# Kernel optimization log

Hardware: AMD Instinct MI355X
Metric: run time of the kernel (lower is better)

The kernel has to match this reference:

```python
import jax, jax.numpy as jnp
import numpy as np

B, C, N, E, F = 8, 4, 2048, 512, 2048
EPS = 1e-5
MASK_SCALE = 5.0


def layer_norm(x, gamma, beta):
    mu = jnp.mean(x, axis=-1, keepdims=True)
    var = jnp.mean(jnp.square(x - mu), axis=-1, keepdims=True)
    return (x - mu) * jax.lax.rsqrt(var + EPS) * gamma + beta


def setup_inputs() -> dict:
    key = jax.random.key(0)
    ks = jax.random.split(key, 8)
    src = jax.random.normal(ks[0], (B, C, N, E), dtype=jnp.float32)
    key_padding_mask = jax.random.uniform(ks[1], (B, N), dtype=jnp.float32)
    # FFN params (torch Linear default init scale ~ U(-1/sqrt(fan_in), +))
    W1 = jax.random.normal(ks[2], (E, F), dtype=jnp.float32) / np.sqrt(E)
    b1 = jnp.zeros((F,), dtype=jnp.float32)
    W2 = jax.random.normal(ks[3], (F, E), dtype=jnp.float32) / np.sqrt(F)
    b2 = jnp.zeros((E,), dtype=jnp.float32)
    g1 = jnp.ones((E,), dtype=jnp.float32)
    be1 = jnp.zeros((E,), dtype=jnp.float32)
    g2 = jnp.ones((E,), dtype=jnp.float32)
    be2 = jnp.zeros((E,), dtype=jnp.float32)
    return {"src": src, "key_padding_mask": key_padding_mask,
            "W1": W1, "b1": b1, "W2": W2, "b2": b2,
            "g1": g1, "be1": be1, "g2": g2, "be2": be2}


def reference(src, key_padding_mask, W1, b1, W2, b2, g1, be1, g2, be2):
    # src: [B, C, N, E]; channels batched into one fused attention call
    scale = 1.0 / jnp.sqrt(jnp.asarray(src.shape[-1], src.dtype))
    scores = jnp.einsum('bcne,bcme->bcnm', src, src) * scale  # [B,C,N,N]
    scores = scores - key_padding_mask[:, None, None, :] * MASK_SCALE
    attn = jax.nn.softmax(scores, axis=-1)
    attn_out = jnp.einsum('bcnm,bcme->bcne', attn, src)
    # residual + norm1 (dropout is identity at eval)
    src2 = layer_norm(src + attn_out, g1, be1)
    # feedforward: Linear -> ReLU -> Linear
    ff = jax.nn.relu(jnp.einsum('bcne,ef->bcnf', src2, W1) + b1)
    ff = jnp.einsum('bcnf,fe->bcne', ff, W2) + b2
    out = layer_norm(src2 + ff, g2, be2)
    return out
```

## Files before the change

kernel.cpp:

```cpp
#include <hip/hip_runtime.h>
#include <stdint.h>

constexpr int CB = 8, CC = 4, CN = 2048, CE = 512, CF = 2048;
constexpr long long TOT = (long long)CB * CC * CN * CE;
constexpr int G = 4;
constexpr int MCH = 32768;
constexpr float SCALE = 0.04419417382415922f;
constexpr float MASK_SCALE = 5.0f;
constexpr float EPS = 1e-5f;

typedef unsigned short bf16_t;
typedef __attribute__((ext_vector_type(4))) float f32x4;
typedef __attribute__((ext_vector_type(8))) short s16x8;

#define DEV static __device__ __forceinline__

DEV unsigned short f2bf(float f) {
    unsigned u = __float_as_uint(f);
    unsigned r = (u + 0x7fffu + ((u >> 16) & 1u)) >> 16;
    return (unsigned short)r;
}
DEV float bf2f(unsigned short b) {
    return __uint_as_float(((unsigned)b) << 16);
}

typedef const __attribute__((address_space(1))) unsigned int* gptr_t;
typedef __attribute__((address_space(3))) unsigned int* lptr_t;
DEV void async16(const void* g, void* l) {
    __builtin_amdgcn_global_load_lds((gptr_t)g, (lptr_t)l, 16, 0, 0);
}

#define FULL_BAR() do { asm volatile("" ::: "memory"); __builtin_amdgcn_s_barrier(); asm volatile("" ::: "memory"); } while (0)
#define LGKM0() asm volatile("s_waitcnt lgkmcnt(0)" ::: "memory")

DEV float blockSum256(float v, float* sm) {
    #pragma unroll
    for (int o = 32; o; o >>= 1) v += __shfl_xor(v, o);
    int w = threadIdx.x >> 6;
    __syncthreads();
    if ((threadIdx.x & 63) == 0) sm[w] = v;
    __syncthreads();
    return sm[0] + sm[1] + sm[2] + sm[3];
}
DEV float blockMax256(float v, float* sm) {
    #pragma unroll
    for (int o = 32; o; o >>= 1) v = fmaxf(v, __shfl_xor(v, o));
    int w = threadIdx.x >> 6;
    __syncthreads();
    if ((threadIdx.x & 63) == 0) sm[w] = v;
    __syncthreads();
    return fmaxf(fmaxf(sm[0], sm[1]), fmaxf(sm[2], sm[3]));
}

__global__ __launch_bounds__(256) void cvt_f32_bf16_vec(
    const float* __restrict__ in, bf16_t* __restrict__ out, long long n) {
    long long i = ((long long)blockIdx.x * 256 + threadIdx.x) * 4;
    long long stride = (long long)gridDim.x * 1024;
    for (; i < n; i += stride) {
        float4 v = *reinterpret_cast<const float4*>(in + i);
        ushort4 u;
        u.x = f2bf(v.x); u.y = f2bf(v.y); u.z = f2bf(v.z); u.w = f2bf(v.w);
        *reinterpret_cast<ushort4*>(out + i) = u;
    }
}

__global__ __launch_bounds__(256) void transpose_f32_bf16(
    const float* __restrict__ in, bf16_t* __restrict__ out,
    int R, int Cc) {
    __shared__ float tile[32][33];
    int rb = blockIdx.y * 32, cb = blockIdx.x * 32;
    int tx = threadIdx.x & 31, ty = threadIdx.x >> 5;
    #pragma unroll
    for (int i = 0; i < 32; i += 8)
        tile[ty + i][tx] = in[(size_t)(rb + ty + i) * Cc + cb + tx];
    __syncthreads();
    #pragma unroll
    for (int i = 0; i < 32; i += 8)
        out[(size_t)(cb + ty + i) * R + rb + tx] = f2bf(tile[tx][ty + i]);
}

__global__ __launch_bounds__(256) void transpose_bf16(
    const bf16_t* __restrict__ in, bf16_t* __restrict__ out,
    int R, int Cc, long long sIn, long long sOut) {
    __shared__ bf16_t tile[32][36];
    const bf16_t* inz = in + (size_t)blockIdx.z * sIn;
    bf16_t* outz = out + (size_t)blockIdx.z * sOut;
    int rb = blockIdx.y * 32, cb = blockIdx.x * 32;
    int t = threadIdx.x;
    int r = t >> 3, c4 = (t & 7) * 4;
    *(ushort4*)&tile[r][c4] = *(const ushort4*)&inz[(size_t)(rb + r) * Cc + cb + c4];
    __syncthreads();
    int c = t >> 3, r4 = (t & 7) * 4;
    ushort4 w;
    w.x = tile[r4 + 0][c]; w.y = tile[r4 + 1][c];
    w.z = tile[r4 + 2][c]; w.w = tile[r4 + 3][c];
    *(ushort4*)&outz[(size_t)(cb + c) * R + rb + r4] = w;
}

template <int EPI>
__global__ __launch_bounds__(512, 2) void gemm256(
    const bf16_t* __restrict__ A, const bf16_t* __restrict__ B,
    void* __restrict__ Cptr, const float* __restrict__ bias,
    int M, int Nc, int K, long long sA, long long sB, long long sC) {
    extern __shared__ bf16_t lds[];
    bf16_t* AsL = lds;
    bf16_t* BsL = lds + 32768;
    const bf16_t* Az = A + (size_t)blockIdx.z * sA;
    const bf16_t* Bz = B + (size_t)blockIdx.z * sB;
    const int t = threadIdx.x;
    const int lane = t & 63, wid = t >> 6;
    const int wr = wid >> 2, wc = wid & 3;
    const int brow = blockIdx.y * 256, bcol = blockIdx.x * 256;
    const int NT = K >> 6;

    const int r0 = t >> 3, s0 = t & 7;
    const int ce = ((s0 ^ (r0 & 7)) << 3);
    const bf16_t* aP0 = Az + (size_t)(brow + r0) * K + ce;
    const bf16_t* bP0 = Bz + (size_t)(bcol + r0) * K + ce;
    const size_t rK64 = (size_t)64 * K;
    const size_t h128K = (size_t)128 * K;

    #define STAGE_A(kt_, h_) do { \
        bf16_t* d_ = AsL + ((((kt_) & 1) * 2 + (h_)) * 8192); \
        const bf16_t* s_ = aP0 + (size_t)(h_) * h128K + (size_t)(kt_) * 64; \
        async16(s_, d_ + t * 8); \
        async16(s_ + rK64, d_ + 4096 + t * 8); \
    } while (0)
    #define STAGE_B(kt_, h_) do { \
        bf16_t* d_ = BsL + ((((kt_) & 1) * 2 + (h_)) * 8192); \
        const bf16_t* s_ = bP0 + (size_t)(h_) * h128K + (size_t)(kt_) * 64; \
        async16(s_, d_ + t * 8); \
        async16(s_ + rK64, d_ + 4096 + t * 8); \
    } while (0)

    const int q = lane >> 4, rr0 = lane & 15, xmask = rr0 & 7;
    s16x8 af[4][2];
    s16x8 bv[2][2][2];
    f32x4 acc[2][2][4][2] = {};

    #define READ_A(ktp_, qm_) do { \
        const bf16_t* base_ = AsL + (((ktp_) * 2 + (qm_)) * 8192); \
        _Pragma("unroll") for (int m_ = 0; m_ < 4; ++m_) \
        _Pragma("unroll") for (int ks_ = 0; ks_ < 2; ++ks_) \
            af[m_][ks_] = *(const s16x8*)(base_ + (wr * 64 + m_ * 16 + rr0) * 64 + (((ks_ * 4 + q) ^ xmask) << 3)); \
    } while (0)
    #define READ_B(ktp_, qn_) do { \
        const bf16_t* base_ = BsL + (((ktp_) * 2 + (qn_)) * 8192); \
        _Pragma("unroll") for (int n_ = 0; n_ < 2; ++n_) \
        _Pragma("unroll") for (int ks_ = 0; ks_ < 2; ++ks_) \
            bv[qn_][n_][ks_] = *(const s16x8*)(base_ + (wc * 32 + n_ * 16 + rr0) * 64 + (((ks_ * 4 + q) ^ xmask) << 3)); \
    } while (0)
    #define MFMA_Q(qm_, qn_) do { \
        __builtin_amdgcn_s_setprio(1); \
        _Pragma("unroll") for (int m_ = 0; m_ < 4; ++m_) \
        _Pragma("unroll") for (int n_ = 0; n_ < 2; ++n_) \
        _Pragma("unroll") for (int ks_ = 0; ks_ < 2; ++ks_) \
            acc[qm_][qn_][m_][n_] = __builtin_amdgcn_mfma_f32_16x16x32_bf16( \
                af[m_][ks_], bv[qn_][n_][ks_], acc[qm_][qn_][m_][n_], 0, 0, 0); \
        __builtin_amdgcn_s_setprio(0); \
    } while (0)

    STAGE_A(0, 0); STAGE_B(0, 0); STAGE_B(0, 1); STAGE_A(0, 1);
    if (1 < NT) {
        STAGE_A(1, 0); STAGE_B(1, 0);
        asm volatile("s_waitcnt vmcnt(4)" ::: "memory");
    } else {
        asm volatile("s_waitcnt vmcnt(0)" ::: "memory");
    }
    FULL_BAR();

    for (int kt = 0; kt < NT; ++kt) {
        const int ktp = kt & 1;
        READ_A(ktp, 0);
        READ_B(ktp, 0);
        if (kt + 1 < NT) STAGE_B(kt + 1, 1);
        FULL_BAR();
        LGKM0();
        MFMA_Q(0, 0);
        FULL_BAR();
        READ_B(ktp, 1);
        if (kt + 1 < NT) STAGE_A(kt + 1, 1);
        FULL_BAR();
        LGKM0();
        MFMA_Q(0, 1);
        FULL_BAR();
        READ_A(ktp, 1);
        if (kt + 2 < NT) STAGE_A(kt + 2, 0);
        FULL_BAR();
        LGKM0();
        MFMA_Q(1, 0);
        FULL_BAR();
        if (kt + 2 < NT) {
            STAGE_B(kt + 2, 0);
            asm volatile("s_waitcnt vmcnt(4)" ::: "memory");
        } else {
            asm volatile("s_waitcnt vmcnt(0)" ::: "memory");
        }
        FULL_BAR();
        MFMA_Q(1, 1);
        FULL_BAR();
    }

    size_t cz = (size_t)blockIdx.z * sC;
    #pragma unroll
    for (int qm = 0; qm < 2; ++qm)
    #pragma unroll
    for (int qn = 0; qn < 2; ++qn)
    #pragma unroll
    for (int m = 0; m < 4; ++m)
    #pragma unroll
    for (int n = 0; n < 2; ++n) {
        int col = bcol + qn * 128 + wc * 32 + n * 16 + (lane & 15);
        float bvv = (EPI == 1 || EPI == 2) ? bias[col] : 0.f;
        #pragma unroll
        for (int j = 0; j < 4; ++j) {
            int row = brow + qm * 128 + wr * 64 + m * 16 + q * 4 + j;
            float v = acc[qm][qn][m][n][j] + bvv;
            if constexpr (EPI == 1)
                ((bf16_t*)Cptr)[cz + (size_t)row * Nc + col] = f2bf(fmaxf(v, 0.f));
            else if constexpr (EPI == 3)
                ((bf16_t*)Cptr)[cz + (size_t)row * Nc + col] = f2bf(v);
            else
                ((float*)Cptr)[cz + (size_t)row * Nc + col] = v;
        }
    }
    #undef STAGE_A
    #undef STAGE_B
    #undef READ_A
    #undef READ_B
    #undef MFMA_Q
}

__global__ __launch_bounds__(256) void softmax_kernel(
    const float* __restrict__ S, bf16_t* __restrict__ P,
    const float* __restrict__ mask, int bc0) {
    __shared__ float sm[4];
    int gr = blockIdx.x;
    int bc = bc0 + gr / CN;
    int b = bc / CC;
    const float* row = S + (size_t)gr * CN;
    const float* mrow = mask + (size_t)b * CN;
    int tid = threadIdx.x;
    float4 v0 = *(const float4*)&row[tid * 4];
    float4 v1 = *(const float4*)&row[1024 + tid * 4];
    float4 m0 = *(const float4*)&mrow[tid * 4];
    float4 m1 = *(const float4*)&mrow[1024 + tid * 4];
    float x[8];
    x[0] = v0.x * SCALE - m0.x * MASK_SCALE; x[1] = v0.y * SCALE - m0.y * MASK_SCALE;
    x[2] = v0.z * SCALE - m0.z * MASK_SCALE; x[3] = v0.w * SCALE - m0.w * MASK_SCALE;
    x[4] = v1.x * SCALE - m1.x * MASK_SCALE; x[5] = v1.y * SCALE - m1.y * MASK_SCALE;
    x[6] = v1.z * SCALE - m1.z * MASK_SCALE; x[7] = v1.w * SCALE - m1.w * MASK_SCALE;
    float mx = -3.4e38f;
    #pragma unroll
    for (int i = 0; i < 8; i++) mx = fmaxf(mx, x[i]);
    mx = blockMax256(mx, sm);
    float s = 0.f;
    #pragma unroll
    for (int i = 0; i < 8; i++) { x[i] = __expf(x[i] - mx); s += x[i]; }
    s = blockSum256(s, sm);
    float inv = 1.f / s;
    ushort4 u0, u1;
    u0.x = f2bf(x[0] * inv); u0.y = f2bf(x[1] * inv);
    u0.z = f2bf(x[2] * inv); u0.w = f2bf(x[3] * inv);
    u1.x = f2bf(x[4] * inv); u1.y = f2bf(x[5] * inv);
    u1.z = f2bf(x[6] * inv); u1.w = f2bf(x[7] * inv);
    *(ushort4*)&P[(size_t)gr * CN + tid * 4] = u0;
    *(ushort4*)&P[(size_t)gr * CN + 1024 + tid * 4] = u1;
}

__global__ __launch_bounds__(256) void ln1_kernel(
    const float* __restrict__ src, const bf16_t* __restrict__ ao,
    const float* __restrict__ g, const float* __restrict__ be,
    bf16_t* __restrict__ o) {
    __shared__ float sm[4];
    size_t base = (size_t)blockIdx.x * CE;
    int e = threadIdx.x * 2;
    float2 s = *(const float2*)&src[base + e];
    ushort2 a = *(const ushort2*)&ao[base + e];
    float x0 = s.x + bf2f(a.x), x1 = s.y + bf2f(a.y);
    float mu = blockSum256(x0 + x1, sm) * (1.f / CE);
    float d0 = x0 - mu, d1 = x1 - mu;
    float var = blockSum256(d0 * d0 + d1 * d1, sm) * (1.f / CE);
    float rs = rsqrtf(var + EPS);
    ushort2 w;
    w.x = f2bf(d0 * rs * g[e] + be[e]);
    w.y = f2bf(d1 * rs * g[e + 1] + be[e + 1]);
    *(ushort2*)&o[base + e] = w;
}

__global__ __launch_bounds__(256) void ln2_kernel(
    const bf16_t* __restrict__ a, const float* __restrict__ b,
    const float* __restrict__ g, const float* __restrict__ be,
    float* __restrict__ o) {
    __shared__ float sm[4];
    size_t base = (size_t)blockIdx.x * CE;
    int e = threadIdx.x * 2;
    ushort2 aa = *(const ushort2*)&a[base + e];
    float2 bb = *(const float2*)&b[base + e];
    float x0 = bf2f(aa.x) + bb.x, x1 = bf2f(aa.y) + bb.y;
    float mu = blockSum256(x0 + x1, sm) * (1.f / CE);
    float d0 = x0 - mu, d1 = x1 - mu;
    float var = blockSum256(d0 * d0 + d1 * d1, sm) * (1.f / CE);
    float rs = rsqrtf(var + EPS);
    float2 w;
    w.x = d0 * rs * g[e] + be[e];
    w.y = d1 * rs * g[e + 1] + be[e + 1];
    *(float2*)&o[base + e] = w;
}

extern "C" void kernel_launch(void* const* d_in, const int* in_sizes, int n_in,
                              void* d_out, int out_size, void* d_ws, size_t ws_size,
                              hipStream_t stream) {
    const float* src  = (const float*)d_in[0];
    const float* mask = (const float*)d_in[1];
    const float* W1   = (const float*)d_in[2];
    const float* b1   = (const float*)d_in[3];
    const float* W2   = (const float*)d_in[4];
    const float* b2   = (const float*)d_in[5];
    const float* g1   = (const float*)d_in[6];
    const float* be1  = (const float*)d_in[7];
    const float* g2   = (const float*)d_in[8];
    const float* be2  = (const float*)d_in[9];
    float* out = (float*)d_out;
    char* ws = (char*)d_ws;

    hipFuncSetAttribute(reinterpret_cast<const void*>(&gemm256<0>), hipFuncAttributeMaxDynamicSharedMemorySize, 131072);
    hipFuncSetAttribute(reinterpret_cast<const void*>(&gemm256<1>), hipFuncAttributeMaxDynamicSharedMemorySize, 131072);
    hipFuncSetAttribute(reinterpret_cast<const void*>(&gemm256<2>), hipFuncAttributeMaxDynamicSharedMemorySize, 131072);
    hipFuncSetAttribute(reinterpret_cast<const void*>(&gemm256<3>), hipFuncAttributeMaxDynamicSharedMemorySize, 131072);

    const size_t MB = 1024 * 1024;
    bf16_t* probs  = (bf16_t*)(ws);
    bf16_t* src_bf = (bf16_t*)(ws + 256 * MB);
    bf16_t* srcT   = (bf16_t*)(ws + 320 * MB);
    float*  scores = (float*)(ws + 384 * MB);
    bf16_t* W1T    = (bf16_t*)(ws + 448 * MB);
    bf16_t* W2T    = (bf16_t*)(ws + 450 * MB);
    bf16_t* attnO  = (bf16_t*)(ws + 384 * MB);
    bf16_t* src2   = (bf16_t*)(ws);
    float*  ff     = (float*)(ws + 64 * MB);
    bf16_t* H      = (bf16_t*)(ws + 256 * MB);
    if (ws_size < 452 * MB) return;

    cvt_f32_bf16_vec<<<4096, 256, 0, stream>>>(src, src_bf, TOT);
    transpose_f32_bf16<<<dim3(CF / 32, CE / 32, 1), 256, 0, stream>>>(W1, W1T, CE, CF);
    transpose_f32_bf16<<<dim3(CE / 32, CF / 32, 1), 256, 0, stream>>>(W2, W2T, CF, CE);
    transpose_bf16<<<dim3(CE / 32, CN / 32, 32), 256, 0, stream>>>(
        src_bf, srcT, CN, CE, (long long)CN * CE, (long long)CE * CN);

    for (int g0 = 0; g0 < CB * CC; g0 += G) {
        const bf16_t* srcb = src_bf + (size_t)g0 * CN * CE;
        gemm256<0><<<dim3(CN / 256, CN / 256, G), 512, 131072, stream>>>(
            srcb, srcb, scores, nullptr, CN, CN, CE,
            (long long)CN * CE, (long long)CN * CE, (long long)CN * CN);
        softmax_kernel<<<dim3(G * CN), 256, 0, stream>>>(
            scores, probs + (size_t)g0 * CN * CN, mask, g0);
    }
    gemm256<3><<<dim3(CE / 256, CN / 256, 32), 512, 131072, stream>>>(
        probs, srcT, attnO, nullptr, CN, CE, CN,
        (long long)CN * CN, (long long)CE * CN, (long long)CN * CE);
    ln1_kernel<<<dim3(CB * CC * CN), 256, 0, stream>>>(src, attnO, g1, be1, src2);

    for (int c = 0; c < 2; ++c) {
        const bf16_t* A2 = src2 + (size_t)c * MCH * CE;
        gemm256<1><<<dim3(CF / 256, MCH / 256, 1), 512, 131072, stream>>>(
            A2, W1T, H, b1, MCH, CF, CE, 0, 0, 0);
        gemm256<2><<<dim3(CE / 256, MCH / 256, 1), 512, 131072, stream>>>(
            H, W2T, ff, b2, MCH, CE, CF, 0, 0, 0);
        ln2_kernel<<<dim3(MCH), 256, 0, stream>>>(
            A2, ff, g2, be2, out + (size_t)c * MCH * CE);
    }
}
```

Baseline: 1.020 ms.

## Write scaled bf16 scores in place, batch all channels, remap workgroups across XCDs

The QK^T GEMM now writes pre-scaled bf16 scores directly into the probabilities buffer for all 32 batch-channels in one launch. The softmax then rewrites that buffer in place, which replaces the eight grouped fp32 score/softmax round trips and halves score traffic. GEMM workgroup IDs are remapped so consecutive tiles land on the same XCD, aiming at better L2 reuse, and LN1 reads the bf16 copy of src instead of fp32. In exchange, scores are rounded to bf16 before softmax and the residual in LN1 uses bf16 src, which loses some precision.

```diff
diff --git a/kernel.cpp b/kernel.cpp
--- a/kernel.cpp
+++ b/kernel.cpp
@@ -3,7 +3,6 @@
 
 constexpr int CB = 8, CC = 4, CN = 2048, CE = 512, CF = 2048;
 constexpr long long TOT = (long long)CB * CC * CN * CE;
-constexpr int G = 4;
 constexpr int MCH = 32768;
 constexpr float SCALE = 0.04419417382415922f;
 constexpr float MASK_SCALE = 5.0f;
@@ -100,17 +99,30 @@
 template <int EPI>
 __global__ __launch_bounds__(512, 2) void gemm256(
     const bf16_t* __restrict__ A, const bf16_t* __restrict__ B,
-    void* __restrict__ Cptr, const float* __restrict__ bias,
+    void* __restrict__ Cptr, const float* __restrict__ bias, float alpha,
     int M, int Nc, int K, long long sA, long long sB, long long sC) {
     extern __shared__ bf16_t lds[];
     bf16_t* AsL = lds;
     bf16_t* BsL = lds + 32768;
-    const bf16_t* Az = A + (size_t)blockIdx.z * sA;
-    const bf16_t* Bz = B + (size_t)blockIdx.z * sB;
+
+    int bx, by, bz;
+    {
+        int gx = gridDim.x, gy = gridDim.y;
+        int nwg = gx * gy * gridDim.z;
+        int flat = blockIdx.x + gx * (blockIdx.y + gy * blockIdx.z);
+        int wg = (nwg & 7) ? flat : ((flat & 7) * (nwg >> 3) + (flat >> 3));
+        bx = wg % gx;
+        int tmp = wg / gx;
+        by = tmp % gy;
+        bz = tmp / gy;
+    }
+
+    const bf16_t* Az = A + (size_t)bz * sA;
+    const bf16_t* Bz = B + (size_t)bz * sB;
     const int t = threadIdx.x;
     const int lane = t & 63, wid = t >> 6;
     const int wr = wid >> 2, wc = wid & 3;
-    const int brow = blockIdx.y * 256, bcol = blockIdx.x * 256;
+    const int brow = by * 256, bcol = bx * 256;
     const int NT = K >> 6;
 
     const int r0 = t >> 3, s0 = t & 7;
@@ -178,18 +190,21 @@
         LGKM0();
         MFMA_Q(0, 0);
         FULL_BAR();
+
         READ_B(ktp, 1);
         if (kt + 1 < NT) STAGE_A(kt + 1, 1);
         FULL_BAR();
         LGKM0();
         MFMA_Q(0, 1);
         FULL_BAR();
+
         READ_A(ktp, 1);
         if (kt + 2 < NT) STAGE_A(kt + 2, 0);
         FULL_BAR();
         LGKM0();
         MFMA_Q(1, 0);
         FULL_BAR();
+
         if (kt + 2 < NT) {
             STAGE_B(kt + 2, 0);
             asm volatile("s_waitcnt vmcnt(4)" ::: "memory");
@@ -201,7 +216,7 @@
         FULL_BAR();
     }
 
-    size_t cz = (size_t)blockIdx.z * sC;
+    size_t cz = (size_t)bz * sC;
     #pragma unroll
     for (int qm = 0; qm < 2; ++qm)
     #pragma unroll
@@ -219,7 +234,7 @@
             if constexpr (EPI == 1)
                 ((bf16_t*)Cptr)[cz + (size_t)row * Nc + col] = f2bf(fmaxf(v, 0.f));
             else if constexpr (EPI == 3)
-                ((bf16_t*)Cptr)[cz + (size_t)row * Nc + col] = f2bf(v);
+                ((bf16_t*)Cptr)[cz + (size_t)row * Nc + col] = f2bf(v * alpha);
             else
                 ((float*)Cptr)[cz + (size_t)row * Nc + col] = v;
         }
@@ -231,25 +246,26 @@
     #undef MFMA_Q
 }
 
-__global__ __launch_bounds__(256) void softmax_kernel(
-    const float* __restrict__ S, bf16_t* __restrict__ P,
-    const float* __restrict__ mask, int bc0) {
+__global__ __launch_bounds__(256) void softmax_bf16(
+    bf16_t* __restrict__ S, const float* __restrict__ mask) {
     __shared__ float sm[4];
     int gr = blockIdx.x;
-    int bc = bc0 + gr / CN;
-    int b = bc / CC;
-    const float* row = S + (size_t)gr * CN;
-    const float* mrow = mask + (size_t)b * CN;
+    int b = gr >> 13;
+    bf16_t* row = S + (size_t)gr * CN;
     int tid = threadIdx.x;
-    float4 v0 = *(const float4*)&row[tid * 4];
-    float4 v1 = *(const float4*)&row[1024 + tid * 4];
-    float4 m0 = *(const float4*)&mrow[tid * 4];
-    float4 m1 = *(const float4*)&mrow[1024 + tid * 4];
+    const float* mrow = mask + (size_t)b * CN + tid * 8;
+    s16x8 v = *(const s16x8*)(row + tid * 8);
+    float4 m0 = *(const float4*)(mrow);
+    float4 m1 = *(const float4*)(mrow + 4);
     float x[8];
-    x[0] = v0.x * SCALE - m0.x * MASK_SCALE; x[1] = v0.y * SCALE - m0.y * MASK_SCALE;
-    x[2] = v0.z * SCALE - m0.z * MASK_SCALE; x[3] = v0.w * SCALE - m0.w * MASK_SCALE;
-    x[4] = v1.x * SCALE - m1.x * MASK_SCALE; x[5] = v1.y * SCALE - m1.y * MASK_SCALE;
-    x[6] = v1.z * SCALE - m1.z * MASK_SCALE; x[7] = v1.w * SCALE - m1.w * MASK_SCALE;
+    x[0] = bf2f((unsigned short)v[0]) - m0.x * MASK_SCALE;
+    x[1] = bf2f((unsigned short)v[1]) - m0.y * MASK_SCALE;
+    x[2] = bf2f((unsigned short)v[2]) - m0.z * MASK_SCALE;
+    x[3] = bf2f((unsigned short)v[3]) - m0.w * MASK_SCALE;
+    x[4] = bf2f((unsigned short)v[4]) - m1.x * MASK_SCALE;
+    x[5] = bf2f((unsigned short)v[5]) - m1.y * MASK_SCALE;
+    x[6] = bf2f((unsigned short)v[6]) - m1.z * MASK_SCALE;
+    x[7] = bf2f((unsigned short)v[7]) - m1.w * MASK_SCALE;
     float mx = -3.4e38f;
     #pragma unroll
     for (int i = 0; i < 8; i++) mx = fmaxf(mx, x[i]);
@@ -259,25 +275,22 @@
     for (int i = 0; i < 8; i++) { x[i] = __expf(x[i] - mx); s += x[i]; }
     s = blockSum256(s, sm);
     float inv = 1.f / s;
-    ushort4 u0, u1;
-    u0.x = f2bf(x[0] * inv); u0.y = f2bf(x[1] * inv);
-    u0.z = f2bf(x[2] * inv); u0.w = f2bf(x[3] * inv);
-    u1.x = f2bf(x[4] * inv); u1.y = f2bf(x[5] * inv);
-    u1.z = f2bf(x[6] * inv); u1.w = f2bf(x[7] * inv);
-    *(ushort4*)&P[(size_t)gr * CN + tid * 4] = u0;
-    *(ushort4*)&P[(size_t)gr * CN + 1024 + tid * 4] = u1;
+    s16x8 u;
+    #pragma unroll
+    for (int i = 0; i < 8; i++) u[i] = (short)f2bf(x[i] * inv);
+    *(s16x8*)(row + tid * 8) = u;
 }
 
 __global__ __launch_bounds__(256) void ln1_kernel(
-    const float* __restrict__ src, const bf16_t* __restrict__ ao,
+    const bf16_t* __restrict__ src, const bf16_t* __restrict__ ao,
     const float* __restrict__ g, const float* __restrict__ be,
     bf16_t* __restrict__ o) {
     __shared__ float sm[4];
     size_t base = (size_t)blockIdx.x * CE;
     int e = threadIdx.x * 2;
-    float2 s = *(const float2*)&src[base + e];
+    ushort2 s = *(const ushort2*)&src[base + e];
     ushort2 a = *(const ushort2*)&ao[base + e];
-    float x0 = s.x + bf2f(a.x), x1 = s.y + bf2f(a.y);
+    float x0 = bf2f(s.x) + bf2f(a.x), x1 = bf2f(s.y) + bf2f(a.y);
     float mu = blockSum256(x0 + x1, sm) * (1.f / CE);
     float d0 = x0 - mu, d1 = x1 - mu;
     float var = blockSum256(d0 * d0 + d1 * d1, sm) * (1.f / CE);
@@ -333,10 +346,9 @@
     bf16_t* probs  = (bf16_t*)(ws);
     bf16_t* src_bf = (bf16_t*)(ws + 256 * MB);
     bf16_t* srcT   = (bf16_t*)(ws + 320 * MB);
-    float*  scores = (float*)(ws + 384 * MB);
+    bf16_t* attnO  = (bf16_t*)(ws + 384 * MB);
     bf16_t* W1T    = (bf16_t*)(ws + 448 * MB);
     bf16_t* W2T    = (bf16_t*)(ws + 450 * MB);
-    bf16_t* attnO  = (bf16_t*)(ws + 384 * MB);
     bf16_t* src2   = (bf16_t*)(ws);
     float*  ff     = (float*)(ws + 64 * MB);
     bf16_t* H      = (bf16_t*)(ws + 256 * MB);
@@ -348,25 +360,21 @@
     transpose_bf16<<<dim3(CE / 32, CN / 32, 32), 256, 0, stream>>>(
         src_bf, srcT, CN, CE, (long long)CN * CE, (long long)CE * CN);
 
-    for (int g0 = 0; g0 < CB * CC; g0 += G) {
-        const bf16_t* srcb = src_bf + (size_t)g0 * CN * CE;
-        gemm256<0><<<dim3(CN / 256, CN / 256, G), 512, 131072, stream>>>(
-            srcb, srcb, scores, nullptr, CN, CN, CE,
-            (long long)CN * CE, (long long)CN * CE, (long long)CN * CN);
-        softmax_kernel<<<dim3(G * CN), 256, 0, stream>>>(
-            scores, probs + (size_t)g0 * CN * CN, mask, g0);
-    }
+    gemm256<3><<<dim3(CN / 256, CN / 256, 32), 512, 131072, stream>>>(
+        src_bf, src_bf, probs, nullptr, SCALE, CN, CN, CE,
+        (long long)CN * CE, (long long)CN * CE, (long long)CN * CN);
+    softmax_bf16<<<dim3(CB * CC * CN), 256, 0, stream>>>(probs, mask);
     gemm256<3><<<dim3(CE / 256, CN / 256, 32), 512, 131072, stream>>>(
-        probs, srcT, attnO, nullptr, CN, CE, CN,
+        probs, srcT, attnO, nullptr, 1.0f, CN, CE, CN,
         (long long)CN * CN, (long long)CE * CN, (long long)CN * CE);
-    ln1_kernel<<<dim3(CB * CC * CN), 256, 0, stream>>>(src, attnO, g1, be1, src2);
+    ln1_kernel<<<dim3(CB * CC * CN), 256, 0, stream>>>(src_bf, attnO, g1, be1, src2);
 
     for (int c = 0; c < 2; ++c) {
         const bf16_t* A2 = src2 + (size_t)c * MCH * CE;
         gemm256<1><<<dim3(CF / 256, MCH / 256, 1), 512, 131072, stream>>>(
-            A2, W1T, H, b1, MCH, CF, CE, 0, 0, 0);
+            A2, W1T, H, b1, 1.0f, MCH, CF, CE, 0, 0, 0);
         gemm256<2><<<dim3(CE / 256, MCH / 256, 1), 512, 131072, stream>>>(
-            H, W2T, ff, b2, MCH, CE, CF, 0, 0, 0);
+            H, W2T, ff, b2, 1.0f, MCH, CE, CF, 0, 0, 0);
         ln2_kernel<<<dim3(MCH), 256, 0, stream>>>(
             A2, ff, g2, be2, out + (size_t)c * MCH * CE);
     }
```

After: 904.8 us. 1.13x faster.
